# Kernel tuning notes

Hardware: AMD Instinct MI355X
Metric: run time of the kernel (lower is better)

The kernel has to match this reference:

```python
import jax, jax.numpy as jnp
import numpy as np

B = 131072
D_IN = 385          # 384-d embedding + 1 correctness feature
D_H = 192           # both trunk layers resolve to max(.,192)=192 per source
Q = 1000            # number of questions
C = 16              # classes per head (uniform padding of per-question heads)


def setup_inputs() -> dict:
    key = jax.random.key(0)
    ks = jax.random.split(key, 9)
    x = jax.random.normal(ks[0], (B, D_IN), dtype=jnp.float32)
    question_ids = jax.random.randint(ks[1], (B,), 0, Q, dtype=jnp.int32)
    is_correct = jax.random.randint(ks[2], (B,), 0, 2, dtype=jnp.int32)
    W1 = jax.random.normal(ks[3], (D_IN, D_H), dtype=jnp.float32) * 0.05
    b1 = jnp.zeros((D_H,), dtype=jnp.float32)
    W2 = jax.random.normal(ks[4], (D_H, D_H), dtype=jnp.float32) * 0.05
    b2 = jnp.zeros((D_H,), dtype=jnp.float32)
    # Head bank: slots [0,Q) = false heads, [Q,2Q) = true heads.
    W_heads = jax.random.normal(ks[5], (2 * Q, C, D_H), dtype=jnp.float32) * 0.05
    b_heads = jax.random.normal(ks[6], (2 * Q, C), dtype=jnp.float32) * 0.05
    return {"x": x, "question_ids": question_ids, "is_correct": is_correct,
            "W1": W1, "b1": b1, "W2": W2, "b2": b2,
            "W_heads": W_heads, "b_heads": b_heads}


def reference(x, question_ids, is_correct, W1, b1, W2, b2, W_heads, b_heads):
    # Shared trunk (eval mode: dropout = identity)
    h = jax.nn.relu(x @ W1 + b1)            # [B, 192]
    feat = jax.nn.relu(h @ W2 + b2)         # [B, 192]
    # Hard routing: pick true or false head for this question.
    Qn = W_heads.shape[0] // 2
    idx = question_ids + is_correct * Qn    # [B]
    Wq = W_heads[idx]                       # [B, C, 192] gather (memory-bound)
    bq = b_heads[idx]                       # [B, C]
    logits = jnp.einsum('bcd,bd->bc', Wq, feat) + bq  # per-sample routed linear
    return logits
```

## Files before the change

### kernel.cpp

```cpp
#include <hip/hip_runtime.h>
#include <hip/hip_bf16.h>
#include <stdint.h>
#include <stddef.h>


typedef short s8v __attribute__((ext_vector_type(8)));
typedef float f4v __attribute__((ext_vector_type(4)));
typedef float f4a __attribute__((ext_vector_type(4), aligned(4)));

typedef const void __attribute__((address_space(1))) *gas1_t;
typedef void __attribute__((address_space(3))) *las3_t;

namespace {
constexpr int kDin = 385;
constexpr int kDh  = 192;
constexpr int kQ   = 1000;
constexpr int kC   = 16;
constexpr int BM   = 64;
constexpr int NT   = 512;
constexpr int NK1  = 13;
constexpr int NK2  = 6;
constexpr int CHUNK = 12 * 64 * 8;
constexpr int H2   = 200;

constexpr size_t WS_W1   = 0;
constexpr size_t WS_W2   = 163840;
constexpr size_t WS_HIST = 245760;
constexpr size_t WS_CUR  = 253952;
constexpr size_t WS_PERM = 262144;
}

__device__ __forceinline__ unsigned short f2bf(float f) {
  unsigned int u = __float_as_uint(f);
  u = u + 0x7fffu + ((u >> 16) & 1u);
  return (unsigned short)(u >> 16);
}

__device__ __forceinline__ unsigned int pk2(float lo, float hi) {
  union { __hip_bfloat162 h2; unsigned int u; } cv;
  cv.h2 = __float22bfloat162_rn(make_float2(lo, hi));
  return cv.u;
}

union s8u { s8v s; unsigned int u[4]; };

__device__ __forceinline__ void swz_one(const float* W, int K, int i,
                                        unsigned short* out) {
  int k = i / kDh;
  int c = i - k * kDh;
  float v = (k < K) ? W[(size_t)k * kDh + c] : 0.f;
  int oi = (k >> 5) * CHUNK + (((c >> 4) * 64 + ((k >> 3) & 3) * 16 + (c & 15)) << 3)
         + (k & 7);
  out[oi] = f2bf(v);
}

__global__ void combo_prep(const int* __restrict__ qid, const int* __restrict__ isc,
                           int B, int nbH,
                           const float* __restrict__ W1, const float* __restrict__ W2,
                           int* __restrict__ hist,
                           unsigned short* __restrict__ W1sw,
                           unsigned short* __restrict__ W2sw) {
  int bid = blockIdx.x;
  if (bid < nbH) {
    int i = bid * 256 + threadIdx.x;
    if (i < B) atomicAdd(&hist[qid[i] + isc[i] * kQ], 1);
  } else if (bid < nbH + 312) {
    swz_one(W1, kDin, (bid - nbH) * 256 + threadIdx.x, W1sw);
  } else {
    swz_one(W2, kDh, (bid - nbH - 312) * 256 + threadIdx.x, W2sw);
  }
}

__global__ __launch_bounds__(256)
void scatter2(const int* __restrict__ qid, const int* __restrict__ isc, int B,
              const int* __restrict__ hist, int* __restrict__ rank_ctr,
              int* __restrict__ perm) {
  __shared__ int sh[2048];
  __shared__ int ssum[256];
  int t = threadIdx.x;
  int4 a = ((const int4*)hist)[t * 2];
  int4 b = ((const int4*)hist)[t * 2 + 1];
  int s1 = a.x + a.y, s2 = s1 + a.z, s3 = s2 + a.w;
  int s4 = s3 + b.x, s5 = s4 + b.y, s6 = s5 + b.z, s7 = s6 + b.w;
  ssum[t] = s7;
  __syncthreads();
  #pragma unroll
  for (int d = 1; d < 256; d <<= 1) {
    int xv = (t >= d) ? ssum[t - d] : 0;
    __syncthreads();
    ssum[t] += xv;
    __syncthreads();
  }
  int base = ssum[t] - s7;
  sh[t * 8 + 0] = base;
  sh[t * 8 + 1] = base + a.x;
  sh[t * 8 + 2] = base + s1;
  sh[t * 8 + 3] = base + s2;
  sh[t * 8 + 4] = base + s3;
  sh[t * 8 + 5] = base + s4;
  sh[t * 8 + 6] = base + s5;
  sh[t * 8 + 7] = base + s6;
  __syncthreads();
  int i = blockIdx.x * 256 + t;
  if (i < B) {
    int h = qid[i] + isc[i] * kQ;
    int pos = sh[h] + atomicAdd(&rank_ctr[h], 1);
    perm[pos] = i;
  }
}

__global__ __launch_bounds__(NT, 8)
void fused_qmlp8(const float* __restrict__ x,
                 const int*   __restrict__ qid,
                 const int*   __restrict__ isc,
                 const float* __restrict__ b1,
                 const float* __restrict__ b2,
                 const float* __restrict__ Wh,
                 const float* __restrict__ bh,
                 const unsigned short* __restrict__ W1sw,
                 const unsigned short* __restrict__ W2sw,
                 const int*   __restrict__ perm,
                 float* __restrict__ out) {
  __shared__ __align__(16) unsigned short hS[BM * H2];
  __shared__ __align__(16) unsigned short bS[CHUNK];
  __shared__ int permS[BM];
  __shared__ int idxS[BM];

  const int tid  = threadIdx.x;
  const int lane = tid & 63, wid = tid >> 6;
  const int m = lane & 15, quad = lane >> 4;
  const int rh = wid >> 1, ch = wid & 1;
  const int row0 = blockIdx.x * BM;

  {
    const char* g = (const char*)W1sw + (size_t)tid * 16;
    char* l = (char*)bS + ((tid >> 6) << 10);
    __builtin_amdgcn_global_load_lds((gas1_t)g, (las3_t)l, 16, 0, 0);
    if (tid < 256)
      __builtin_amdgcn_global_load_lds((gas1_t)(g + 8192), (las3_t)(l + 8192),
                                       16, 0, 0);
  }
  if (tid < BM) {
    int p = perm[row0 + tid];
    permS[tid] = p;
    idxS[tid] = qid[p] + isc[p] * kQ;
  }
  __syncthreads();

  const float* px = x + (size_t)permS[rh * 16 + m] * kDin;

  f4v acc[6];
  #pragma unroll
  for (int t = 0; t < 6; ++t) acc[t] = (f4v){0.f, 0.f, 0.f, 0.f};

  f4a c0 = *(const f4a*)(px + quad * 8);
  f4a c1 = *(const f4a*)(px + quad * 8 + 4);
  float tl = 0.f;

  #pragma unroll
  for (int kk = 0; kk < NK1; ++kk) {
    s8v a;
    if (kk < NK1 - 1) {
      s8u ua;
      ua.u[0] = pk2(c0[0], c0[1]); ua.u[1] = pk2(c0[2], c0[3]);
      ua.u[2] = pk2(c1[0], c1[1]); ua.u[3] = pk2(c1[2], c1[3]);
      a = ua.s;
    } else {
      a = (s8v){0,0,0,0,0,0,0,0};
      a[0] = (short)f2bf(tl);
    }

    #pragma unroll
    for (int t = 0; t < 6; ++t) {
      s8v b = *(const s8v*)&bS[((ch * 6 + t) * 64 + lane) * 8];
      acc[t] = __builtin_amdgcn_mfma_f32_16x16x32_bf16(a, b, acc[t], 0, 0, 0);
    }
    __syncthreads();

    {
      const unsigned short* np = (kk < NK1 - 1)
          ? W1sw + (size_t)(kk + 1) * CHUNK : W2sw;
      const char* g = (const char*)np + (size_t)tid * 16;
      char* l = (char*)bS + ((tid >> 6) << 10);
      __builtin_amdgcn_global_load_lds((gas1_t)g, (las3_t)l, 16, 0, 0);
      if (tid < 256)
        __builtin_amdgcn_global_load_lds((gas1_t)(g + 8192), (las3_t)(l + 8192),
                                         16, 0, 0);
    }
    if (kk < NK1 - 2) {
      c0 = *(const f4a*)(px + (kk + 1) * 32 + quad * 8);
      c1 = *(const f4a*)(px + (kk + 1) * 32 + quad * 8 + 4);
    } else if (kk == NK1 - 2) {
      tl = (quad == 0) ? px[384] : 0.f;
    }
    if (kk == NK1 - 1) {
      #pragma unroll
      for (int t = 0; t < 6; ++t) {
        int c = ch * 96 + t * 16 + m;
        float bb = b1[c];
        #pragma unroll
        for (int r4 = 0; r4 < 4; ++r4) {
          int r = rh * 16 + quad * 4 + r4;
          float v0 = acc[t][r4] + bb;
          hS[r * H2 + c] = f2bf(v0 > 0.f ? v0 : 0.f);
          acc[t][r4] = 0.f;
        }
      }
    }
    __syncthreads();
  }

  const int ar0 = (rh * 16 + m) * H2;
  #pragma unroll
  for (int k2 = 0; k2 < NK2; ++k2) {
    s8v a = *(const s8v*)&hS[ar0 + k2 * 32 + quad * 8];
    #pragma unroll
    for (int t = 0; t < 6; ++t) {
      s8v b = *(const s8v*)&bS[((ch * 6 + t) * 64 + lane) * 8];
      acc[t] = __builtin_amdgcn_mfma_f32_16x16x32_bf16(a, b, acc[t], 0, 0, 0);
    }
    __syncthreads();
    if (k2 < NK2 - 1) {
      const char* g = (const char*)(W2sw + (size_t)(k2 + 1) * CHUNK)
                    + (size_t)tid * 16;
      char* l = (char*)bS + ((tid >> 6) << 10);
      __builtin_amdgcn_global_load_lds((gas1_t)g, (las3_t)l, 16, 0, 0);
      if (tid < 256)
        __builtin_amdgcn_global_load_lds((gas1_t)(g + 8192), (las3_t)(l + 8192),
                                         16, 0, 0);
    } else {
      #pragma unroll
      for (int t = 0; t < 6; ++t) {
        int c = ch * 96 + t * 16 + m;
        float bb = b2[c];
        #pragma unroll
        for (int r4 = 0; r4 < 4; ++r4) {
          int r = rh * 16 + quad * 4 + r4;
          float v0 = acc[t][r4] + bb;
          hS[r * H2 + c] = f2bf(v0 > 0.f ? v0 : 0.f);
        }
      }
    }
    __syncthreads();
  }

  {
    const int w16 = rh * 16;
    const int hm = idxS[w16 + m];
    unsigned rem = 0xFFFFu;
    int runIdx = 0;
    while (rem) {
      int r0 = (int)__builtin_ctz(rem);
      int h = idxS[w16 + r0];
      unsigned long long bal = __ballot(hm == h);
      unsigned mask16 = (unsigned)(bal & 0xFFFFu);
      rem &= ~mask16;
      if ((runIdx & 1) == ch) {
        const float* wq = Wh + ((size_t)h * kC + m) * kDh + quad * 8;
        f4v acch = (f4v){0.f, 0.f, 0.f, 0.f};
        #pragma unroll
        for (int kk = 0; kk < 6; ++kk) {
          float4 wlo = *(const float4*)(wq + kk * 32);
          float4 whi = *(const float4*)(wq + kk * 32 + 4);
          s8u ub;
          ub.u[0] = pk2(wlo.x, wlo.y);
          ub.u[1] = pk2(wlo.z, wlo.w);
          ub.u[2] = pk2(whi.x, whi.y);
          ub.u[3] = pk2(whi.z, whi.w);
          s8v bfr = ub.s;
          s8v afr = *(const s8v*)&hS[(w16 + m) * H2 + kk * 32 + quad * 8];
          if (hm != h) afr = (s8v){0,0,0,0,0,0,0,0};
          acch = __builtin_amdgcn_mfma_f32_16x16x32_bf16(afr, bfr, acch, 0, 0, 0);
        }
        float bhv = bh[(size_t)h * kC + m];
        #pragma unroll
        for (int reg = 0; reg < 4; ++reg) {
          int r = quad * 4 + reg;
          if ((mask16 >> r) & 1u)
            out[(size_t)permS[w16 + r] * kC + m] = acch[reg] + bhv;
        }
      }
      runIdx++;
    }
  }
}

extern "C" void kernel_launch(void* const* d_in, const int* in_sizes, int n_in,
                              void* d_out, int out_size, void* d_ws, size_t ws_size,
                              hipStream_t stream) {
  const float* x  = (const float*)d_in[0];
  const int*   qd = (const int*)  d_in[1];
  const int*   ic = (const int*)  d_in[2];
  const float* W1 = (const float*)d_in[3];
  const float* b1 = (const float*)d_in[4];
  const float* W2 = (const float*)d_in[5];
  const float* b2 = (const float*)d_in[6];
  const float* Wh = (const float*)d_in[7];
  const float* bh = (const float*)d_in[8];
  float* out = (float*)d_out;

  char* ws = (char*)d_ws;
  unsigned short* W1sw = (unsigned short*)(ws + WS_W1);
  unsigned short* W2sw = (unsigned short*)(ws + WS_W2);
  int* hist = (int*)(ws + WS_HIST);
  int* rank = (int*)(ws + WS_CUR);
  int* perm = (int*)(ws + WS_PERM);

  int B = in_sizes[1];
  int nbH = (B + 255) / 256;

  hipMemsetAsync(hist, 0, 4096 * sizeof(int), stream);
  combo_prep<<<nbH + 312 + 144, 256, 0, stream>>>(qd, ic, B, nbH, W1, W2,
                                                  hist, W1sw, W2sw);
  scatter2<<<(B + 255) / 256, 256, 0, stream>>>(qd, ic, B, hist, rank, perm);

  fused_qmlp8<<<B / BM, NT, 0, stream>>>(x, qd, ic, b1, b2, Wh, bh,
                                         W1sw, W2sw, perm, out);
}
```

Before: 392.0 us.

## Split fused trunk/head kernel into trunk and sorted head passes via feature buffer

When the workspace is large enough, the single fused kernel is split in two. The trunk kernel reads x rows contiguously in natural order and writes bf16 features to a global buffer. The head kernel then gathers those features in question-sorted order and applies the routed heads. This replaces the permuted, scattered reads of 385-float x rows with coalesced trunk reads, at the cost of an extra 48MB feature write and read plus one more launch. The old fused path is kept as a fallback when the workspace is too small.

```diff
diff --git a/kernel.cpp b/kernel.cpp
--- a/kernel.cpp
+++ b/kernel.cpp
@@ -28,6 +28,15 @@
 constexpr size_t WS_HIST = 245760;
 constexpr size_t WS_CUR  = 253952;
 constexpr size_t WS_PERM = 262144;
+
+constexpr size_t WB_FEAT = 0;
+constexpr size_t WB_W1   = 50331648;
+constexpr size_t WB_W2   = WB_W1 + 159744;
+constexpr size_t WB_HIST = WB_W2 + 73728;
+constexpr size_t WB_CUR  = WB_HIST + 8192;
+constexpr size_t WB_PERM = WB_CUR + 8192;
+constexpr size_t WB_NEED = WB_PERM + 524288;
+constexpr size_t WS_SANE_MAX = (1ull << 36);
 }
 
 __device__ __forceinline__ unsigned short f2bf(float f) {
@@ -106,6 +115,203 @@
     int h = qid[i] + isc[i] * kQ;
     int pos = sh[h] + atomicAdd(&rank_ctr[h], 1);
     perm[pos] = i;
+  }
+}
+
+__global__ __launch_bounds__(NT, 8)
+void trunk_k(const float* __restrict__ x,
+             const float* __restrict__ b1,
+             const float* __restrict__ b2,
+             const unsigned short* __restrict__ W1sw,
+             const unsigned short* __restrict__ W2sw,
+             unsigned short* __restrict__ featG) {
+  __shared__ __align__(16) unsigned short hS[BM * H2];
+  __shared__ __align__(16) unsigned short bS[CHUNK];
+
+  const int tid  = threadIdx.x;
+  const int lane = tid & 63, wid = tid >> 6;
+  const int m = lane & 15, quad = lane >> 4;
+  const int rh = wid >> 1, ch = wid & 1;
+  const int row0 = blockIdx.x * BM;
+
+  {
+    const char* g = (const char*)W1sw + (size_t)tid * 16;
+    char* l = (char*)bS + ((tid >> 6) << 10);
+    __builtin_amdgcn_global_load_lds((gas1_t)g, (las3_t)l, 16, 0, 0);
+    if (tid < 256)
+      __builtin_amdgcn_global_load_lds((gas1_t)(g + 8192), (las3_t)(l + 8192),
+                                       16, 0, 0);
+  }
+
+  const float* px = x + (size_t)(row0 + rh * 16 + m) * kDin;
+
+  f4v acc[6];
+  #pragma unroll
+  for (int t = 0; t < 6; ++t) acc[t] = (f4v){0.f, 0.f, 0.f, 0.f};
+
+  f4a c0 = *(const f4a*)(px + quad * 8);
+  f4a c1 = *(const f4a*)(px + quad * 8 + 4);
+  float tl = 0.f;
+  __syncthreads();
+
+  #pragma unroll
+  for (int kk = 0; kk < NK1; ++kk) {
+    s8v a;
+    if (kk < NK1 - 1) {
+      s8u ua;
+      ua.u[0] = pk2(c0[0], c0[1]); ua.u[1] = pk2(c0[2], c0[3]);
+      ua.u[2] = pk2(c1[0], c1[1]); ua.u[3] = pk2(c1[2], c1[3]);
+      a = ua.s;
+    } else {
+      a = (s8v){0,0,0,0,0,0,0,0};
+      a[0] = (short)f2bf(tl);
+    }
+
+    #pragma unroll
+    for (int t = 0; t < 6; ++t) {
+      s8v b = *(const s8v*)&bS[((ch * 6 + t) * 64 + lane) * 8];
+      acc[t] = __builtin_amdgcn_mfma_f32_16x16x32_bf16(a, b, acc[t], 0, 0, 0);
+    }
+    __syncthreads();
+
+    {
+      const unsigned short* np = (kk < NK1 - 1)
+          ? W1sw + (size_t)(kk + 1) * CHUNK : W2sw;
+      const char* g = (const char*)np + (size_t)tid * 16;
+      char* l = (char*)bS + ((tid >> 6) << 10);
+      __builtin_amdgcn_global_load_lds((gas1_t)g, (las3_t)l, 16, 0, 0);
+      if (tid < 256)
+        __builtin_amdgcn_global_load_lds((gas1_t)(g + 8192), (las3_t)(l + 8192),
+                                         16, 0, 0);
+    }
+    if (kk < NK1 - 2) {
+      c0 = *(const f4a*)(px + (kk + 1) * 32 + quad * 8);
+      c1 = *(const f4a*)(px + (kk + 1) * 32 + quad * 8 + 4);
+    } else if (kk == NK1 - 2) {
+      tl = (quad == 0) ? px[384] : 0.f;
+    }
+    if (kk == NK1 - 1) {
+      #pragma unroll
+      for (int t = 0; t < 6; ++t) {
+        int c = ch * 96 + t * 16 + m;
+        float bb = b1[c];
+        #pragma unroll
+        for (int r4 = 0; r4 < 4; ++r4) {
+          int r = rh * 16 + quad * 4 + r4;
+          float v0 = acc[t][r4] + bb;
+          hS[r * H2 + c] = f2bf(v0 > 0.f ? v0 : 0.f);
+          acc[t][r4] = 0.f;
+        }
+      }
+    }
+    __syncthreads();
+  }
+
+  const int ar0 = (rh * 16 + m) * H2;
+  #pragma unroll
+  for (int k2 = 0; k2 < NK2; ++k2) {
+    s8v a = *(const s8v*)&hS[ar0 + k2 * 32 + quad * 8];
+    #pragma unroll
+    for (int t = 0; t < 6; ++t) {
+      s8v b = *(const s8v*)&bS[((ch * 6 + t) * 64 + lane) * 8];
+      acc[t] = __builtin_amdgcn_mfma_f32_16x16x32_bf16(a, b, acc[t], 0, 0, 0);
+    }
+    __syncthreads();
+    if (k2 < NK2 - 1) {
+      const char* g = (const char*)(W2sw + (size_t)(k2 + 1) * CHUNK)
+                    + (size_t)tid * 16;
+      char* l = (char*)bS + ((tid >> 6) << 10);
+      __builtin_amdgcn_global_load_lds((gas1_t)g, (las3_t)l, 16, 0, 0);
+      if (tid < 256)
+        __builtin_amdgcn_global_load_lds((gas1_t)(g + 8192), (las3_t)(l + 8192),
+                                         16, 0, 0);
+    } else {
+      #pragma unroll
+      for (int t = 0; t < 6; ++t) {
+        int c = ch * 96 + t * 16 + m;
+        float bb = b2[c];
+        #pragma unroll
+        for (int r4 = 0; r4 < 4; ++r4) {
+          int r = rh * 16 + quad * 4 + r4;
+          float v0 = acc[t][r4] + bb;
+          hS[r * H2 + c] = f2bf(v0 > 0.f ? v0 : 0.f);
+        }
+      }
+    }
+    __syncthreads();
+  }
+
+  #pragma unroll
+  for (int j = 0; j < 3; ++j) {
+    int e = tid + j * NT;
+    int row = e / 24, c8 = e - row * 24;
+    *(s8v*)&featG[(size_t)(row0 + row) * kDh + c8 * 8] =
+        *(const s8v*)&hS[row * H2 + c8 * 8];
+  }
+}
+
+__global__ __launch_bounds__(NT, 8)
+void head_k(const int* __restrict__ qid, const int* __restrict__ isc,
+            const float* __restrict__ Wh, const float* __restrict__ bh,
+            const unsigned short* __restrict__ featG,
+            const int* __restrict__ perm, float* __restrict__ out) {
+  __shared__ int permS[BM];
+  __shared__ int idxS[BM];
+
+  const int tid  = threadIdx.x;
+  const int lane = tid & 63, wid = tid >> 6;
+  const int m = lane & 15, quad = lane >> 4;
+  const int rh = wid >> 1, ch = wid & 1;
+  const int row0 = blockIdx.x * BM;
+
+  if (tid < BM) {
+    int p = perm[row0 + tid];
+    permS[tid] = p;
+    idxS[tid] = qid[p] + isc[p] * kQ;
+  }
+  __syncthreads();
+
+  const int w16 = rh * 16;
+  const unsigned short* fp = featG + (size_t)permS[w16 + m] * kDh + quad * 8;
+  s8v f[6];
+  #pragma unroll
+  for (int kk = 0; kk < 6; ++kk) f[kk] = *(const s8v*)(fp + kk * 32);
+
+  const int hm = idxS[w16 + m];
+  const s8v zf = (s8v){0,0,0,0,0,0,0,0};
+  unsigned rem = 0xFFFFu;
+  int runIdx = 0;
+  while (rem) {
+    int r0 = (int)__builtin_ctz(rem);
+    int h = idxS[w16 + r0];
+    unsigned long long bal = __ballot(hm == h);
+    unsigned mask16 = (unsigned)(bal & 0xFFFFu);
+    rem &= ~mask16;
+    if ((runIdx & 1) == ch) {
+      bool valid = (hm == h);
+      const float* wq = Wh + ((size_t)h * kC + m) * kDh + quad * 8;
+      f4v acch = (f4v){0.f, 0.f, 0.f, 0.f};
+      #pragma unroll
+      for (int kk = 0; kk < 6; ++kk) {
+        float4 wlo = *(const float4*)(wq + kk * 32);
+        float4 whi = *(const float4*)(wq + kk * 32 + 4);
+        s8u ub;
+        ub.u[0] = pk2(wlo.x, wlo.y);
+        ub.u[1] = pk2(wlo.z, wlo.w);
+        ub.u[2] = pk2(whi.x, whi.y);
+        ub.u[3] = pk2(whi.z, whi.w);
+        s8v afr = valid ? f[kk] : zf;
+        acch = __builtin_amdgcn_mfma_f32_16x16x32_bf16(afr, ub.s, acch, 0, 0, 0);
+      }
+      float bhv = bh[(size_t)h * kC + m];
+      #pragma unroll
+      for (int reg = 0; reg < 4; ++reg) {
+        int r = quad * 4 + reg;
+        if ((mask16 >> r) & 1u)
+          out[(size_t)permS[w16 + r] * kC + m] = acch[reg] + bhv;
+      }
+    }
+    runIdx++;
   }
 }
 
@@ -267,10 +473,9 @@
           ub.u[1] = pk2(wlo.z, wlo.w);
           ub.u[2] = pk2(whi.x, whi.y);
           ub.u[3] = pk2(whi.z, whi.w);
-          s8v bfr = ub.s;
           s8v afr = *(const s8v*)&hS[(w16 + m) * H2 + kk * 32 + quad * 8];
           if (hm != h) afr = (s8v){0,0,0,0,0,0,0,0};
-          acch = __builtin_amdgcn_mfma_f32_16x16x32_bf16(afr, bfr, acch, 0, 0, 0);
+          acch = __builtin_amdgcn_mfma_f32_16x16x32_bf16(afr, ub.s, acch, 0, 0, 0);
         }
         float bhv = bh[(size_t)h * kC + m];
         #pragma unroll
@@ -300,20 +505,38 @@
   float* out = (float*)d_out;
 
   char* ws = (char*)d_ws;
-  unsigned short* W1sw = (unsigned short*)(ws + WS_W1);
-  unsigned short* W2sw = (unsigned short*)(ws + WS_W2);
-  int* hist = (int*)(ws + WS_HIST);
-  int* rank = (int*)(ws + WS_CUR);
-  int* perm = (int*)(ws + WS_PERM);
-
   int B = in_sizes[1];
   int nbH = (B + 255) / 256;
 
-  hipMemsetAsync(hist, 0, 4096 * sizeof(int), stream);
-  combo_prep<<<nbH + 312 + 144, 256, 0, stream>>>(qd, ic, B, nbH, W1, W2,
-                                                  hist, W1sw, W2sw);
-  scatter2<<<(B + 255) / 256, 256, 0, stream>>>(qd, ic, B, hist, rank, perm);
-
-  fused_qmlp8<<<B / BM, NT, 0, stream>>>(x, qd, ic, b1, b2, Wh, bh,
-                                         W1sw, W2sw, perm, out);
-}
+  const bool big = (d_ws != nullptr) && (ws_size >= WB_NEED)
+                 && (ws_size < WS_SANE_MAX);
+
+  if (big) {
+    unsigned short* featG = (unsigned short*)(ws + WB_FEAT);
+    unsigned short* W1sw  = (unsigned short*)(ws + WB_W1);
+    unsigned short* W2sw  = (unsigned short*)(ws + WB_W2);
+    int* hist = (int*)(ws + WB_HIST);
+    int* rank = (int*)(ws + WB_CUR);
+    int* perm = (int*)(ws + WB_PERM);
+
+    hipMemsetAsync(hist, 0, 4096 * sizeof(int), stream);
+    combo_prep<<<nbH + 312 + 144, 256, 0, stream>>>(qd, ic, B, nbH, W1, W2,
+                                                    hist, W1sw, W2sw);
+    scatter2<<<(B + 255) / 256, 256, 0, stream>>>(qd, ic, B, hist, rank, perm);
+    trunk_k<<<B / BM, NT, 0, stream>>>(x, b1, b2, W1sw, W2sw, featG);
+    head_k<<<B / BM, NT, 0, stream>>>(qd, ic, Wh, bh, featG, perm, out);
+  } else {
+    unsigned short* W1sw = (unsigned short*)(ws + WS_W1);
+    unsigned short* W2sw = (unsigned short*)(ws + WS_W2);
+    int* hist = (int*)(ws + WS_HIST);
+    int* rank = (int*)(ws + WS_CUR);
+    int* perm = (int*)(ws + WS_PERM);
+
+    hipMemsetAsync(hist, 0, 4096 * sizeof(int), stream);
+    combo_prep<<<nbH + 312 + 144, 256, 0, stream>>>(qd, ic, B, nbH, W1, W2,
+                                                    hist, W1sw, W2sw);
+    scatter2<<<(B + 255) / 256, 256, 0, stream>>>(qd, ic, B, hist, rank, perm);
+    fused_qmlp8<<<B / BM, NT, 0, stream>>>(x, qd, ic, b1, b2, Wh, bh,
+                                           W1sw, W2sw, perm, out);
+  }
+}
```

After: 419.6 us. +7.0%, slower.
